# Optimization experiments

Hardware: AMD Instinct MI355X
Metric: run time of the kernel (lower is better)

## Reference

```python
import jax, jax.numpy as jnp
import numpy as np

RES_SIZE = 64
SR = 24000
MIN_FREQ = 10.0
MAX_FREQ = 12000.0
DECAY_FACTOR = 0.999
HIGH_FREQ_DECAY = 0.6


def _build_kernels():
    # Deterministic complex resonator bank from __init__ (registered buffer).
    freqs = np.logspace(np.log10(MIN_FREQ), np.log10(MAX_FREQ), RES_SIZE)
    decays = np.linspace(DECAY_FACTOR, HIGH_FREQ_DECAY, RES_SIZE)
    k_len = int(1.0 * SR)  # 24000
    t = np.arange(k_len)
    thetas = 2 * np.pi * freqs / SR
    eig = decays * np.exp(1j * thetas)  # (64,)
    kernels = eig[:, None] ** t[None, :]  # (64, 24000) complex
    kernels /= np.abs(kernels).sum(axis=1, keepdims=True)
    return kernels.astype(np.complex64)


def setup_inputs() -> dict:
    key = jax.random.key(0)
    audio = jax.random.normal(key, (8, 48000), dtype=jnp.float32)
    k = _build_kernels()
    return {
        "audio": audio,
        "kernels_re": jnp.asarray(k.real, dtype=jnp.float32),
        "kernels_im": jnp.asarray(k.imag, dtype=jnp.float32),
    }


def reference(audio, kernels_re, kernels_im):
    # audio: (B, T) float32; kernels: (C=64, K=24000) complex64 (as re/im pair)
    kernels = (kernels_re + 1j * kernels_im).astype(jnp.complex64)
    T = audio.shape[-1]
    K = kernels.shape[-1]
    n_fft = T + K - 1
    audio_c = audio.astype(jnp.complex64)

    ker_f = jnp.fft.fft(kernels, n=n_fft, axis=-1)[None, :, :]  # (1, C, n_fft)

    # forward-direction convolution
    sig_f = jnp.fft.fft(audio_c[:, None, :], n=n_fft, axis=-1)  # (B, 1, n_fft)
    out_f = jnp.fft.ifft(sig_f * ker_f, axis=-1)[..., :T]        # (B, C, T)

    # backward-direction convolution (time-reversed input, then re-reversed)
    sig_b = jnp.fft.fft(audio_c[:, ::-1][:, None, :], n=n_fft, axis=-1)
    out_b = jnp.fft.ifft(sig_b * ker_f, axis=-1)[..., :T][..., ::-1]

    # (B, 4*C, T): [RealF, ImagF, RealB, ImagB]
    return jnp.concatenate(
        [out_f.real, out_f.imag, out_b.real, out_b.imag], axis=1
    ).astype(jnp.float32)
```

## Files before the change

kernel.cpp:

```cpp
#include <hip/hip_runtime.h>

#define BATCH   8
#define NCH     64
#define TLEN    48000
#define KLEN    24000
#define NDIR    2
#define NCHUNK  25
#define LCHUNK  1920
#define NTILE   30
#define NTASK   (BATCH*NDIR*NCHUNK*NCH)
#define NSEQ    (BATCH*NDIR*NCH)

#define WS_EIG_OFF  (2 * NTASK * sizeof(float2))

__device__ __forceinline__ void cmuld(double& ar, double& ai, double br, double bi) {
    double r = ar * br - ai * bi;
    double i = ar * bi + ai * br;
    ar = r; ai = i;
}

__global__ __launch_bounds__(64) void pass0_eig(double* __restrict__ eig_out) {
    int c = threadIdx.x;
    if (c >= NCH) return;
    double fc   = (double)c / 63.0;
    double dec  = 0.999 + (0.6 - 0.999) * fc;
    double lf   = 1.0 + (4.0791812460476247 - 1.0) * fc;
    double f    = pow(10.0, lf);
    double th   = 2.0 * 3.14159265358979323846 * f / 24000.0;
    eig_out[2 * c]     = dec * cos(th);
    eig_out[2 * c + 1] = dec * sin(th);
}

__global__ __launch_bounds__(256) void pass_a(const float* __restrict__ audio,
                                              const double* __restrict__ eig,
                                              float2* __restrict__ s_out) {
    int lane = threadIdx.x & 63;
    int task = blockIdx.x * 4 + (threadIdx.x >> 6);
    int c     = task & 63;
    int tmp   = task >> 6;
    int chunk = tmp % NCHUNK;
    int bd    = tmp / NCHUNK;
    int d     = bd & 1;
    int b     = bd >> 1;

    double er = eig[2 * c], ei = eig[2 * c + 1];
    double Er[7], Ei[7];
    Er[0] = er; Ei[0] = ei;
    #pragma unroll
    for (int s = 1; s < 7; ++s) {
        double r = Er[s - 1], i = Ei[s - 1];
        Er[s] = r * r - i * i; Ei[s] = 2.0 * r * i;
    }
    int n = 63 - lane;
    double qr = 1.0, qi = 0.0;
    #pragma unroll
    for (int s = 0; s < 6; ++s)
        if (n & (1 << s)) cmuld(qr, qi, Er[s], Ei[s]);
    float qrf = (float)qr, qif = (float)qi;
    float e64r = (float)Er[6], e64i = (float)Ei[6];

    const float* ab = audio + b * TLEN;
    int base = chunk * LCHUNK;
    float accr = 0.f, acci = 0.f;
    for (int j = 0; j < NTILE; ++j) {
        int u = base + j * 64 + lane;
        int t = d ? (TLEN - 1 - u) : u;
        float a = ab[t];
        float tr = a * qrf, ti = a * qif;
        #pragma unroll
        for (int s = 0; s < 6; ++s) {
            tr += __shfl_xor(tr, 1 << s, 64);
            ti += __shfl_xor(ti, 1 << s, 64);
        }
        float nr = e64r * accr - e64i * acci + tr;
        float ni = e64r * acci + e64i * accr + ti;
        accr = nr; acci = ni;
    }
    if (lane == 0) s_out[task] = make_float2(accr, acci);
}

__global__ __launch_bounds__(256) void pass_b(const float2* __restrict__ s_in,
                                              const double* __restrict__ eig,
                                              float2* __restrict__ S_out) {
    int tid = blockIdx.x * 256 + threadIdx.x;
    if (tid >= NSEQ) return;
    int c  = tid & 63;
    int bd = tid >> 6;

    double er = eig[2 * c], ei = eig[2 * c + 1];
    double E64r = er, E64i = ei;
    #pragma unroll
    for (int s = 0; s < 6; ++s) {
        double r = E64r, i = E64i;
        E64r = r * r - i * i; E64i = 2.0 * r * i;
    }
    double lr = 1.0, li = 0.0, br = E64r, bi = E64i;
    int e = NTILE;
    while (e) {
        if (e & 1) cmuld(lr, li, br, bi);
        double r = br, i = bi;
        br = r * r - i * i; bi = 2.0 * r * i;
        e >>= 1;
    }
    double Sr = 0.0, Si = 0.0;
    for (int i = 0; i < NCHUNK; ++i) {
        int idx = (bd * NCHUNK + i) * NCH + c;
        S_out[idx] = make_float2((float)Sr, (float)Si);
        float2 s = s_in[idx];
        double nr = lr * Sr - li * Si + (double)s.x;
        double ni = lr * Si + li * Sr + (double)s.y;
        Sr = nr; Si = ni;
    }
}

__global__ __launch_bounds__(256) void pass_c(const float* __restrict__ audio,
                                              const float* __restrict__ kre,
                                              const double* __restrict__ eig,
                                              const float2* __restrict__ S_in,
                                              float* __restrict__ out) {
    int lane = threadIdx.x & 63;
    int task = blockIdx.x * 4 + (threadIdx.x >> 6);
    int c     = task & 63;
    int tmp   = task >> 6;
    int chunk = tmp % NCHUNK;
    int bd    = tmp / NCHUNK;
    int d     = bd & 1;
    int b     = bd >> 1;

    double er = eig[2 * c], ei = eig[2 * c + 1];
    double Er[7], Ei[7];
    Er[0] = er; Ei[0] = ei;
    #pragma unroll
    for (int s = 1; s < 7; ++s) {
        double r = Er[s - 1], i = Ei[s - 1];
        Er[s] = r * r - i * i; Ei[s] = 2.0 * r * i;
    }
    float esr[6], esi[6];
    #pragma unroll
    for (int s = 0; s < 6; ++s) { esr[s] = (float)Er[s]; esi[s] = (float)Ei[s]; }
    int n = lane + 1;
    double pr = 1.0, pi = 0.0;
    #pragma unroll
    for (int s = 0; s < 7; ++s)
        if (n & (1 << s)) cmuld(pr, pi, Er[s], Ei[s]);
    float prf = (float)pr, pif = (float)pi;

    float g = kre[c * KLEN];
    float2 S0 = S_in[task];
    float Sr = S0.x, Si = S0.y;

    const float* ab = audio + b * TLEN;
    float* outR = out + (size_t)((b * 256) + (d ? 128 : 0) + c) * TLEN;
    float* outI = outR + (size_t)64 * TLEN;
    int base = chunk * LCHUNK;

    for (int j = 0; j < NTILE; ++j) {
        int u = base + j * 64 + lane;
        int t = d ? (TLEN - 1 - u) : u;
        float a = ab[t];
        float yr = a, yi = 0.f;
        #pragma unroll
        for (int s = 0; s < 6; ++s) {
            float vr = __shfl_up(yr, (unsigned)(1 << s), 64);
            float vi = __shfl_up(yi, (unsigned)(1 << s), 64);
            bool ok = lane >= (1 << s);
            vr = ok ? vr : 0.f;
            vi = ok ? vi : 0.f;
            yr += esr[s] * vr - esi[s] * vi;
            yi += esr[s] * vi + esi[s] * vr;
        }
        yr += prf * Sr - pif * Si;
        yi += prf * Si + pif * Sr;
        outR[t] = g * yr;
        outI[t] = g * yi;
        Sr = __shfl(yr, 63, 64);
        Si = __shfl(yi, 63, 64);
    }
}

extern "C" void kernel_launch(void* const* d_in, const int* in_sizes, int n_in,
                              void* d_out, int out_size, void* d_ws, size_t ws_size,
                              hipStream_t stream) {
    const float* audio = (const float*)d_in[0];
    const float* kre   = (const float*)d_in[1];
    float* out         = (float*)d_out;

    float2* ws_s  = (float2*)d_ws;
    float2* ws_S  = ws_s + NTASK;
    double* ws_eig = (double*)((char*)d_ws + WS_EIG_OFF);

    pass0_eig<<<1, 64, 0, stream>>>(ws_eig);
    pass_a<<<NTASK / 4, 256, 0, stream>>>(audio, ws_eig, ws_s);
    pass_b<<<(NSEQ + 255) / 256, 256, 0, stream>>>(ws_s, ws_eig, ws_S);
    pass_c<<<NTASK / 4, 256, 0, stream>>>(audio, kre, ws_eig, ws_S, out);
}
```

Before: 543.0 us.

## Restructure chunked recurrence scan with lane-per-channel pass A and float4 pass C

Shrinks chunks to 256 samples and reorganizes pass A so each lane owns one channel and runs a serial two-step recurrence over the chunk, with no cross-lane reductions. Pass C now handles one 256-sample chunk per wavefront, with each lane processing 4 samples via float4 loads and stores plus a single shuffle scan. The intent is to remove the shuffle-heavy 30-tile loops and produce wider, coalesced output writes. In exchange, pass B's serial carry chain grows from 25 to 188 steps, and more of the eigenvalue-power math runs in float, which may reduce accuracy.

Result: faster. 453.4 us (-16.5%).

```diff
diff --git a/kernel.cpp b/kernel.cpp
--- a/kernel.cpp
+++ b/kernel.cpp
@@ -5,28 +5,22 @@
 #define TLEN    48000
 #define KLEN    24000
 #define NDIR    2
-#define NCHUNK  25
-#define LCHUNK  1920
-#define NTILE   30
-#define NTASK   (BATCH*NDIR*NCHUNK*NCH)
-#define NSEQ    (BATCH*NDIR*NCH)
+#define CHUNK   256
+#define NCHUNK  188
+#define NBD     (BATCH*NDIR)
+#define NTASK_A (NBD*NCHUNK)
+#define NTASK_C (NTASK_A*NCH)
 
-#define WS_EIG_OFF  (2 * NTASK * sizeof(float2))
-
-__device__ __forceinline__ void cmuld(double& ar, double& ai, double br, double bi) {
-    double r = ar * br - ai * bi;
-    double i = ar * bi + ai * br;
-    ar = r; ai = i;
-}
+#define WS_EIG_OFF ((size_t)NTASK_C * sizeof(float2))
 
 __global__ __launch_bounds__(64) void pass0_eig(double* __restrict__ eig_out) {
     int c = threadIdx.x;
     if (c >= NCH) return;
-    double fc   = (double)c / 63.0;
-    double dec  = 0.999 + (0.6 - 0.999) * fc;
-    double lf   = 1.0 + (4.0791812460476247 - 1.0) * fc;
-    double f    = pow(10.0, lf);
-    double th   = 2.0 * 3.14159265358979323846 * f / 24000.0;
+    double fc  = (double)c / 63.0;
+    double dec = 0.999 + (0.6 - 0.999) * fc;
+    double lf  = 1.0 + (4.0791812460476247 - 1.0) * fc;
+    double f   = pow(10.0, lf);
+    double th  = 2.0 * 3.14159265358979323846 * f / 24000.0;
     eig_out[2 * c]     = dec * cos(th);
     eig_out[2 * c + 1] = dec * sin(th);
 }
@@ -36,77 +30,50 @@
                                               float2* __restrict__ s_out) {
     int lane = threadIdx.x & 63;
     int task = blockIdx.x * 4 + (threadIdx.x >> 6);
-    int c     = task & 63;
-    int tmp   = task >> 6;
-    int chunk = tmp % NCHUNK;
-    int bd    = tmp / NCHUNK;
-    int d     = bd & 1;
-    int b     = bd >> 1;
+    int chunk = task % NCHUNK;
+    int bd    = task / NCHUNK;
+    int d = bd & 1, b = bd >> 1;
+    int c = lane;
 
-    double er = eig[2 * c], ei = eig[2 * c + 1];
-    double Er[7], Ei[7];
-    Er[0] = er; Ei[0] = ei;
-    #pragma unroll
-    for (int s = 1; s < 7; ++s) {
-        double r = Er[s - 1], i = Ei[s - 1];
-        Er[s] = r * r - i * i; Ei[s] = 2.0 * r * i;
-    }
-    int n = 63 - lane;
-    double qr = 1.0, qi = 0.0;
-    #pragma unroll
-    for (int s = 0; s < 6; ++s)
-        if (n & (1 << s)) cmuld(qr, qi, Er[s], Ei[s]);
-    float qrf = (float)qr, qif = (float)qi;
-    float e64r = (float)Er[6], e64i = (float)Ei[6];
+    float er = (float)eig[2 * c], ei = (float)eig[2 * c + 1];
+    float E2r = er * er - ei * ei, E2i = 2.f * er * ei;
 
     const float* ab = audio + b * TLEN;
-    int base = chunk * LCHUNK;
-    float accr = 0.f, acci = 0.f;
-    for (int j = 0; j < NTILE; ++j) {
-        int u = base + j * 64 + lane;
-        int t = d ? (TLEN - 1 - u) : u;
-        float a = ab[t];
-        float tr = a * qrf, ti = a * qif;
-        #pragma unroll
-        for (int s = 0; s < 6; ++s) {
-            tr += __shfl_xor(tr, 1 << s, 64);
-            ti += __shfl_xor(ti, 1 << s, 64);
-        }
-        float nr = e64r * accr - e64i * acci + tr;
-        float ni = e64r * acci + e64i * accr + ti;
-        accr = nr; acci = ni;
+    int base = chunk * CHUNK;
+    int len  = min(CHUNK, TLEN - base);
+
+    float sr = 0.f, si = 0.f;
+    for (int t = 0; t < len; t += 2) {
+        int u0 = base + t, u1 = base + t + 1;
+        float x0 = ab[d ? (TLEN - 1 - u0) : u0];
+        float x1 = ab[d ? (TLEN - 1 - u1) : u1];
+        float wr = er * x0 + x1;
+        float wi = ei * x0;
+        float nr = E2r * sr - E2i * si + wr;
+        float ni = E2r * si + E2i * sr + wi;
+        sr = nr; si = ni;
     }
-    if (lane == 0) s_out[task] = make_float2(accr, acci);
+    s_out[task * NCH + c] = make_float2(sr, si);
 }
 
-__global__ __launch_bounds__(256) void pass_b(const float2* __restrict__ s_in,
-                                              const double* __restrict__ eig,
-                                              float2* __restrict__ S_out) {
+__global__ __launch_bounds__(256) void pass_b(float2* __restrict__ buf,
+                                              const double* __restrict__ eig) {
     int tid = blockIdx.x * 256 + threadIdx.x;
-    if (tid >= NSEQ) return;
+    if (tid >= NBD * NCH) return;
     int c  = tid & 63;
     int bd = tid >> 6;
 
     double er = eig[2 * c], ei = eig[2 * c + 1];
-    double E64r = er, E64i = ei;
+    double lr = er, li = ei;
     #pragma unroll
-    for (int s = 0; s < 6; ++s) {
-        double r = E64r, i = E64i;
-        E64r = r * r - i * i; E64i = 2.0 * r * i;
-    }
-    double lr = 1.0, li = 0.0, br = E64r, bi = E64i;
-    int e = NTILE;
-    while (e) {
-        if (e & 1) cmuld(lr, li, br, bi);
-        double r = br, i = bi;
-        br = r * r - i * i; bi = 2.0 * r * i;
-        e >>= 1;
-    }
+    for (int s = 0; s < 8; ++s) { double r = lr, i = li; lr = r * r - i * i; li = 2.0 * r * i; }
+
     double Sr = 0.0, Si = 0.0;
+    #pragma unroll 4
     for (int i = 0; i < NCHUNK; ++i) {
         int idx = (bd * NCHUNK + i) * NCH + c;
-        S_out[idx] = make_float2((float)Sr, (float)Si);
-        float2 s = s_in[idx];
+        float2 s = buf[idx];
+        buf[idx] = make_float2((float)Sr, (float)Si);
         double nr = lr * Sr - li * Si + (double)s.x;
         double ni = lr * Si + li * Sr + (double)s.y;
         Sr = nr; Si = ni;
@@ -124,57 +91,79 @@
     int tmp   = task >> 6;
     int chunk = tmp % NCHUNK;
     int bd    = tmp / NCHUNK;
-    int d     = bd & 1;
-    int b     = bd >> 1;
+    int d = bd & 1, b = bd >> 1;
 
-    double er = eig[2 * c], ei = eig[2 * c + 1];
-    double Er[7], Ei[7];
-    Er[0] = er; Ei[0] = ei;
+    float Er[8], Ei[8];
+    Er[0] = (float)eig[2 * c]; Ei[0] = (float)eig[2 * c + 1];
     #pragma unroll
-    for (int s = 1; s < 7; ++s) {
-        double r = Er[s - 1], i = Ei[s - 1];
-        Er[s] = r * r - i * i; Ei[s] = 2.0 * r * i;
+    for (int s = 1; s < 8; ++s) {
+        float r = Er[s - 1], i = Ei[s - 1];
+        Er[s] = r * r - i * i; Ei[s] = 2.f * r * i;
     }
-    float esr[6], esi[6];
+    float Qr = 1.f, Qi = 0.f;
     #pragma unroll
-    for (int s = 0; s < 6; ++s) { esr[s] = (float)Er[s]; esi[s] = (float)Ei[s]; }
-    int n = lane + 1;
-    double pr = 1.0, pi = 0.0;
-    #pragma unroll
-    for (int s = 0; s < 7; ++s)
-        if (n & (1 << s)) cmuld(pr, pi, Er[s], Ei[s]);
-    float prf = (float)pr, pif = (float)pi;
+    for (int s = 0; s < 6; ++s) {
+        float fr = Er[s + 2], fi = Ei[s + 2];
+        float nr = Qr * fr - Qi * fi, ni = Qr * fi + Qi * fr;
+        bool bit = (lane >> s) & 1;
+        Qr = bit ? nr : Qr; Qi = bit ? ni : Qi;
+    }
+    float e1r = Er[0], e1i = Ei[0];
+    float e2r = Er[1], e2i = Ei[1];
+    float e3r = e1r * e2r - e1i * e2i, e3i = e1r * e2i + e1i * e2r;
+    float e4r = Er[2], e4i = Ei[2];
 
-    float g = kre[c * KLEN];
-    float2 S0 = S_in[task];
-    float Sr = S0.x, Si = S0.y;
+    float  g  = kre[c * KLEN];
+    float2 Sp = S_in[task];
 
     const float* ab = audio + b * TLEN;
-    float* outR = out + (size_t)((b * 256) + (d ? 128 : 0) + c) * TLEN;
+    int base = chunk * CHUNK;
+    int u    = base + 4 * lane;
+    bool act = u < TLEN;
+
+    float4 x;
+    if (act) {
+        if (!d) x = *(const float4*)(ab + u);
+        else { float4 r = *(const float4*)(ab + (TLEN - 4 - u)); x = make_float4(r.w, r.z, r.y, r.x); }
+    } else x = make_float4(0.f, 0.f, 0.f, 0.f);
+
+    float z0r = x.x,                          z0i = 0.f;
+    float z1r = e1r * z0r + x.y,              z1i = e1i * z0r;
+    float z2r = e1r * z1r - e1i * z1i + x.z,  z2i = e1r * z1i + e1i * z1r;
+    float z3r = e1r * z2r - e1i * z2i + x.w,  z3i = e1r * z2i + e1i * z2r;
+
+    float Sr = z3r, Si = z3i;
+    #pragma unroll
+    for (int s = 0; s < 6; ++s) {
+        float vr = __shfl_up(Sr, (unsigned)(1 << s), 64);
+        float vi = __shfl_up(Si, (unsigned)(1 << s), 64);
+        bool ok = lane >= (1 << s);
+        vr = ok ? vr : 0.f; vi = ok ? vi : 0.f;
+        float fr = Er[s + 2], fi = Ei[s + 2];
+        Sr += fr * vr - fi * vi;
+        Si += fr * vi + fi * vr;
+    }
+    float Cr = __shfl_up(Sr, 1u, 64), Ci = __shfl_up(Si, 1u, 64);
+    if (lane == 0) { Cr = 0.f; Ci = 0.f; }
+    float Dr = Cr + Qr * Sp.x - Qi * Sp.y;
+    float Di = Ci + Qr * Sp.y + Qi * Sp.x;
+
+    float y0r = z0r + e1r * Dr - e1i * Di, y0i = z0i + e1r * Di + e1i * Dr;
+    float y1r = z1r + e2r * Dr - e2i * Di, y1i = z1i + e2r * Di + e2i * Dr;
+    float y2r = z2r + e3r * Dr - e3i * Di, y2i = z2i + e3r * Di + e3i * Dr;
+    float y3r = z3r + e4r * Dr - e4i * Di, y3i = z3i + e4r * Di + e4i * Dr;
+
+    float* outR = out + (size_t)(b * 256 + d * 128 + c) * TLEN;
     float* outI = outR + (size_t)64 * TLEN;
-    int base = chunk * LCHUNK;
-
-    for (int j = 0; j < NTILE; ++j) {
-        int u = base + j * 64 + lane;
-        int t = d ? (TLEN - 1 - u) : u;
-        float a = ab[t];
-        float yr = a, yi = 0.f;
-        #pragma unroll
-        for (int s = 0; s < 6; ++s) {
-            float vr = __shfl_up(yr, (unsigned)(1 << s), 64);
-            float vi = __shfl_up(yi, (unsigned)(1 << s), 64);
-            bool ok = lane >= (1 << s);
-            vr = ok ? vr : 0.f;
-            vi = ok ? vi : 0.f;
-            yr += esr[s] * vr - esi[s] * vi;
-            yi += esr[s] * vi + esi[s] * vr;
+    if (act) {
+        if (!d) {
+            *(float4*)(outR + u) = make_float4(g * y0r, g * y1r, g * y2r, g * y3r);
+            *(float4*)(outI + u) = make_float4(g * y0i, g * y1i, g * y2i, g * y3i);
+        } else {
+            int p = TLEN - 4 - u;
+            *(float4*)(outR + p) = make_float4(g * y3r, g * y2r, g * y1r, g * y0r);
+            *(float4*)(outI + p) = make_float4(g * y3i, g * y2i, g * y1i, g * y0i);
         }
-        yr += prf * Sr - pif * Si;
-        yi += prf * Si + pif * Sr;
-        outR[t] = g * yr;
-        outI[t] = g * yi;
-        Sr = __shfl(yr, 63, 64);
-        Si = __shfl(yi, 63, 64);
     }
 }
 
@@ -185,12 +174,11 @@
     const float* kre   = (const float*)d_in[1];
     float* out         = (float*)d_out;
 
-    float2* ws_s  = (float2*)d_ws;
-    float2* ws_S  = ws_s + NTASK;
+    float2* ws_buf = (float2*)d_ws;
     double* ws_eig = (double*)((char*)d_ws + WS_EIG_OFF);
 
     pass0_eig<<<1, 64, 0, stream>>>(ws_eig);
-    pass_a<<<NTASK / 4, 256, 0, stream>>>(audio, ws_eig, ws_s);
-    pass_b<<<(NSEQ + 255) / 256, 256, 0, stream>>>(ws_s, ws_eig, ws_S);
-    pass_c<<<NTASK / 4, 256, 0, stream>>>(audio, kre, ws_eig, ws_S, out);
+    pass_a<<<NTASK_A / 4, 256, 0, stream>>>(audio, ws_eig, ws_buf);
+    pass_b<<<(NBD * NCH + 255) / 256, 256, 0, stream>>>(ws_buf, ws_eig);
+    pass_c<<<NTASK_C / 4, 256, 0, stream>>>(audio, kre, ws_eig, ws_buf, out);
 }
```
